# Optimization experiments

Hardware: AMD Instinct MI355X
Metric: run time of the kernel (lower is better)

Reference implementation:

```python
import jax, jax.numpy as jnp
import numpy as np

WBITS = 4   # weight bits (symmetric signed)
ABITS = 4   # activation bits (unsigned, [0,1])
CBITS = 4   # partial-sum quantization bits
ARRAY = 128 # crossbar array size (input-dim tile)
BN_EPS = 1e-5


def ste_round(x):
    # straight-through estimator round (identity gradient)
    return x + jax.lax.stop_gradient(jnp.round(x) - x)


def setup_inputs() -> dict:
    key = jax.random.key(0)
    k1, k2 = jax.random.split(key)
    B, FIN, FOUT = 65536, 256, 256
    x = jax.random.uniform(k1, (B, FIN), dtype=jnp.float32)        # quantized-act range [0,1]
    weight = jax.random.normal(k2, (FOUT, FIN), dtype=jnp.float32) * 0.05
    gamma = jnp.ones((FOUT,), jnp.float32)
    beta = jnp.zeros((FOUT,), jnp.float32)
    return {"x": x, "weight": weight, "gamma": gamma, "beta": beta}


def reference(x, weight, gamma, beta):
    qmax_w = 2 ** (WBITS - 1) - 1          # 7
    qmax_a = 2 ** ABITS - 1                # 15

    # --- symmetric weight quantization to WBITS (integer levels) ---
    scale_w = jnp.max(jnp.abs(weight)) / qmax_w
    w_int = ste_round(jnp.clip(weight / scale_w, -qmax_w, qmax_w))  # [Fout, Fin]

    # --- unsigned activation quantization to ABITS (integer levels) ---
    x_int = ste_round(jnp.clip(x, 0.0, 1.0) * qmax_a)               # [B, Fin]

    # --- crossbar-tiled integer matmul with partial-sum quantization ---
    B, Fin = x.shape
    Fout = weight.shape[0]
    T = Fin // ARRAY
    xt = x_int.reshape(B, T, ARRAY)          # [B, T, A]
    wt = w_int.reshape(Fout, T, ARRAY)       # [Fout, T, A]
    psum = jnp.einsum('bta,ota->bto', xt, wt)  # integer partial sums, [B, T, Fout]

    # quantize each partial sum to CBITS levels over the full tile dynamic range
    pmax = float(ARRAY * qmax_a * qmax_w)
    step = (2.0 * pmax) / (2 ** CBITS - 1)
    psum_q = ste_round(psum / step) * step

    acc = psum_q.sum(axis=1) * (scale_w / qmax_a)   # dequantized linear output [B, Fout]

    # --- BatchNorm1d (training mode: batch statistics) ---
    mu = acc.mean(axis=0)
    var = acc.var(axis=0)
    y = (acc - mu) * jax.lax.rsqrt(var + BN_EPS) * gamma + beta

    # --- quantized clipped-ReLU activation to ABITS ---
    out = ste_round(jnp.clip(y, 0.0, 1.0) * qmax_a) / qmax_a
    return out
```

## Files before the change

kernel.cpp:

```cpp
#include <hip/hip_runtime.h>
#include <cstdint>
#include <cstddef>

typedef int   v4i __attribute__((ext_vector_type(4)));
typedef float v4f __attribute__((ext_vector_type(4)));

static constexpr int NREP = 16;

static constexpr size_t WQ_OFF    = 0;
static constexpr size_t STATS_OFF = 65536;
static constexpr size_t SCALE_OFF = STATS_OFF + NREP*512*4;
static constexpr size_t AB_OFF    = SCALE_OFF + 64;
static constexpr size_t SBUF_OFF  = 131072 + 2048;
static constexpr size_t WS_NEEDED = SBUF_OFF + (size_t)65536 * 256;
static constexpr size_t ZERO_BYTES = NREP*512*4 + 64;

__device__ __forceinline__ int rhe1792(int p) {
    unsigned u = (unsigned)(p + 17024);
    unsigned v = u >> 8;
    unsigned d = (v * 147u) >> 10;
    int q = (int)d - 9;
    unsigned tie = (unsigned)(((u & 255u) | (v - 7u * d)) == 0u);
    q -= (int)(tie & ((unsigned)q & 1u));
    return q;
}

__global__ void k_maxabs(const float* __restrict__ w, unsigned* scalebits) {
    int idx = blockIdx.x * 256 + threadIdx.x;
    float4 f = ((const float4*)w)[idx];
    float m = fmaxf(fmaxf(fabsf(f.x), fabsf(f.y)), fmaxf(fabsf(f.z), fabsf(f.w)));
    #pragma unroll
    for (int s = 32; s > 0; s >>= 1) m = fmaxf(m, __shfl_xor(m, s, 64));
    if ((threadIdx.x & 63) == 0) atomicMax(scalebits, __float_as_uint(m));
}

__global__ void k_wquant(const float* __restrict__ w, const unsigned* __restrict__ scalebits,
                         signed char* __restrict__ wq) {
    int idx = blockIdx.x * 256 + threadIdx.x;
    float scale = __uint_as_float(*scalebits) / 7.0f;
    float4 f = ((const float4*)w)[idx];
    int q0 = (int)rintf(fminf(fmaxf(f.x / scale, -7.f), 7.f));
    int q1 = (int)rintf(fminf(fmaxf(f.y / scale, -7.f), 7.f));
    int q2 = (int)rintf(fminf(fmaxf(f.z / scale, -7.f), 7.f));
    int q3 = (int)rintf(fminf(fmaxf(f.w / scale, -7.f), 7.f));
    ((int*)wq)[idx] = (q0 & 255) | ((q1 & 255) << 8) | ((q2 & 255) << 16) | ((q3 & 255) << 24);
}

template <typename ST>
__global__ __launch_bounds__(256, 3) void k_gemm(
    const float* __restrict__ x, const signed char* __restrict__ wq,
    ST* __restrict__ sbuf, int* __restrict__ stats)
{
    __shared__ __align__(16) signed char ldsx[2][16 * 272];
    const int tid  = threadIdx.x;
    const int lane = tid & 63;
    const int wv   = tid >> 6;
    const int obase = wv * 64;
    const int lr = lane & 15, quad = lane >> 4;

    v4i wf[4][4];
    #pragma unroll
    for (int ot = 0; ot < 4; ++ot)
        #pragma unroll
        for (int kt = 0; kt < 4; ++kt)
            wf[ot][kt] = *(const v4i*)(wq + (size_t)(obase + ot * 16 + lr) * 256 + kt * 64 + quad * 16);

    int ssum[4] = {0, 0, 0, 0};
    int ssq[4]  = {0, 0, 0, 0};

    const int r = tid >> 4, g = tid & 15;
    const int ITER = 4;
    const size_t rb0 = (size_t)blockIdx.x * (16 * ITER);

    v4f f[4];
    {
        const v4f* xr = (const v4f*)(x + (rb0 + r) * 256);
        #pragma unroll
        for (int j = 0; j < 4; ++j) f[j] = __builtin_nontemporal_load(&xr[j * 16 + g]);
    }

    for (int it = 0; it < ITER; ++it) {
        signed char* lb = ldsx[it & 1];
        #pragma unroll
        for (int j = 0; j < 4; ++j) {
            int b0 = (int)rintf(fminf(fmaxf(f[j][0], 0.f), 1.f) * 15.f);
            int b1 = (int)rintf(fminf(fmaxf(f[j][1], 0.f), 1.f) * 15.f);
            int b2 = (int)rintf(fminf(fmaxf(f[j][2], 0.f), 1.f) * 15.f);
            int b3 = (int)rintf(fminf(fmaxf(f[j][3], 0.f), 1.f) * 15.f);
            *(int*)(lb + r * 272 + j * 64 + g * 4) = b0 | (b1 << 8) | (b2 << 16) | (b3 << 24);
        }
        __syncthreads();
        if (it + 1 < ITER) {
            const v4f* xr = (const v4f*)(x + (rb0 + (it + 1) * 16 + r) * 256);
            #pragma unroll
            for (int j = 0; j < 4; ++j) f[j] = __builtin_nontemporal_load(&xr[j * 16 + g]);
        }
        v4i a[4];
        #pragma unroll
        for (int kt = 0; kt < 4; ++kt)
            a[kt] = *(const v4i*)(lb + lr * 272 + kt * 64 + quad * 16);
        const size_t rowbase = rb0 + (size_t)it * 16;
        #pragma unroll
        for (int ot = 0; ot < 4; ++ot) {
            v4i acc0 = {0, 0, 0, 0}, acc1 = {0, 0, 0, 0};
            acc0 = __builtin_amdgcn_mfma_i32_16x16x64_i8(a[0], wf[ot][0], acc0, 0, 0, 0);
            acc0 = __builtin_amdgcn_mfma_i32_16x16x64_i8(a[1], wf[ot][1], acc0, 0, 0, 0);
            acc1 = __builtin_amdgcn_mfma_i32_16x16x64_i8(a[2], wf[ot][2], acc1, 0, 0, 0);
            acc1 = __builtin_amdgcn_mfma_i32_16x16x64_i8(a[3], wf[ot][3], acc1, 0, 0, 0);
            const int ocol = obase + ot * 16 + lr;
            ST* sp = sbuf + (rowbase + quad * 4) * 256 + ocol;
            #pragma unroll
            for (int e = 0; e < 4; ++e) {
                int s = rhe1792(acc0[e]) + rhe1792(acc1[e]);
                ssum[ot] += s;
                ssq[ot]  += s * s;
                sp[(size_t)e * 256] = (ST)s;
            }
        }
    }
    int* st = stats + (blockIdx.x & (NREP - 1)) * 512;
    #pragma unroll
    for (int ot = 0; ot < 4; ++ot) {
        int v = ssum[ot], u = ssq[ot];
        v += __shfl_xor(v, 16, 64); v += __shfl_xor(v, 32, 64);
        u += __shfl_xor(u, 16, 64); u += __shfl_xor(u, 32, 64);
        if (quad == 0) {
            atomicAdd(&st[obase + ot * 16 + lr], v);
            atomicAdd(&st[256 + obase + ot * 16 + lr], u);
        }
    }
}

__global__ void k_stats(const int* __restrict__ stats, const unsigned* __restrict__ scalebits,
                        const float* __restrict__ gamma, const float* __restrict__ beta,
                        float2* __restrict__ AB)
{
    int o = threadIdx.x;
    int s = 0, q = 0;
    #pragma unroll
    for (int rr = 0; rr < NREP; ++rr) {
        s += stats[rr * 512 + o];
        q += stats[rr * 512 + 256 + o];
    }
    float scale_w = __uint_as_float(*scalebits) / 7.0f;
    float t = scale_w / 15.0f;
    double Cs = 1792.0 * (double)t;
    const double N = 65536.0;
    double mean_s = (double)s / N;
    double var_s  = (double)q / N - mean_s * mean_s;
    double var    = Cs * Cs * var_s;
    double inv    = 1.0 / sqrt(var + 1e-5);
    double A = Cs * inv * (double)gamma[o];
    double B = (double)beta[o] - Cs * mean_s * inv * (double)gamma[o];
    AB[o] = make_float2((float)A, (float)B);
}

template <typename LT>
__global__ __launch_bounds__(256) void k_out(const LT* sbuf, const float2* __restrict__ AB,
                                             float* out)
{
    const int tid = threadIdx.x;
    const int o0 = (tid * 4) & 255;
    const float4 ab01 = *(const float4*)((const float*)AB + 2 * o0);
    const float4 ab23 = *(const float4*)((const float*)AB + 2 * o0 + 4);
    const size_t base = (size_t)blockIdx.x * 1024 + tid;
    #pragma unroll
    for (int j = 0; j < 4; ++j) {
        const size_t F4 = base + (size_t)j * 256;
        float v0, v1, v2, v3;
        if constexpr (sizeof(LT) == 1) {
            int sv = ((const int*)sbuf)[F4];
            v0 = (float)((sv << 24) >> 24);
            v1 = (float)((sv << 16) >> 24);
            v2 = (float)((sv << 8) >> 24);
            v3 = (float)(sv >> 24);
        } else {
            v4f fl = ((const v4f*)sbuf)[F4];
            v0 = fl[0]; v1 = fl[1]; v2 = fl[2]; v3 = fl[3];
        }
        float y0 = rintf(fminf(fmaxf(v0 * ab01.x + ab01.y, 0.f), 1.f) * 15.f);
        float y1 = rintf(fminf(fmaxf(v1 * ab01.z + ab01.w, 0.f), 1.f) * 15.f);
        float y2 = rintf(fminf(fmaxf(v2 * ab23.x + ab23.y, 0.f), 1.f) * 15.f);
        float y3 = rintf(fminf(fmaxf(v3 * ab23.z + ab23.w, 0.f), 1.f) * 15.f);
        const float inv15 = 0.066666666666666666f;
        v4f o = { y0 * inv15, y1 * inv15, y2 * inv15, y3 * inv15 };
        __builtin_nontemporal_store(o, (v4f*)out + F4);
    }
}

extern "C" void kernel_launch(void* const* d_in, const int* in_sizes, int n_in,
                              void* d_out, int out_size, void* d_ws, size_t ws_size,
                              hipStream_t stream)
{
    const float* x     = (const float*)d_in[0];
    const float* w     = (const float*)d_in[1];
    const float* gamma = (const float*)d_in[2];
    const float* beta  = (const float*)d_in[3];
    float* out = (float*)d_out;
    char* ws = (char*)d_ws;

    signed char* wq        = (signed char*)(ws + WQ_OFF);
    int*         stats     = (int*)(ws + STATS_OFF);
    unsigned*    scalebits = (unsigned*)(ws + SCALE_OFF);
    float2*      AB        = (float2*)(ws + AB_OFF);

    hipMemsetAsync(ws + STATS_OFF, 0, ZERO_BYTES, stream);
    k_maxabs<<<dim3(64), dim3(256), 0, stream>>>(w, scalebits);
    k_wquant<<<dim3(64), dim3(256), 0, stream>>>(w, scalebits, wq);

    if (ws_size >= WS_NEEDED) {
        signed char* sbuf = (signed char*)(ws + SBUF_OFF);
        k_gemm<signed char><<<dim3(1024), dim3(256), 0, stream>>>(x, wq, sbuf, stats);
        k_stats<<<dim3(1), dim3(256), 0, stream>>>(stats, scalebits, gamma, beta, AB);
        k_out<signed char><<<dim3(4096), dim3(256), 0, stream>>>(sbuf, AB, out);
    } else {
        k_gemm<float><<<dim3(1024), dim3(256), 0, stream>>>(x, wq, out, stats);
        k_stats<<<dim3(1), dim3(256), 0, stream>>>(stats, scalebits, gamma, beta, AB);
        k_out<float><<<dim3(4096), dim3(256), 0, stream>>>(out, AB, out);
    }
}
```

Baseline: 146.4 us.

## Drop memset via in-kernel zeroing and front-load all x loads in GEMM

Replaces the hipMemsetAsync and the atomicMax scale reduction with per-block partial maxima that k_maxabs writes. k_maxabs also zeroes the stats buffer, and k_wquant and k_stats each reduce the 64 partials themselves. The GEMM kernel now issues all 16 float4 loads for its 64 rows up front and quantizes them into one 64-row LDS tile with a single barrier, replacing the double-buffered 16-row pipeline. This removes one stream operation and the per-iteration syncs, at the cost of more registers and LDS per block, which could lower occupancy.

```diff
diff --git a/kernel.cpp b/kernel.cpp
--- a/kernel.cpp
+++ b/kernel.cpp
@@ -9,11 +9,10 @@
 
 static constexpr size_t WQ_OFF    = 0;
 static constexpr size_t STATS_OFF = 65536;
-static constexpr size_t SCALE_OFF = STATS_OFF + NREP*512*4;
-static constexpr size_t AB_OFF    = SCALE_OFF + 64;
+static constexpr size_t PART_OFF  = STATS_OFF + NREP*512*4;
+static constexpr size_t AB_OFF    = PART_OFF + 256;
 static constexpr size_t SBUF_OFF  = 131072 + 2048;
 static constexpr size_t WS_NEEDED = SBUF_OFF + (size_t)65536 * 256;
-static constexpr size_t ZERO_BYTES = NREP*512*4 + 64;
 
 __device__ __forceinline__ int rhe1792(int p) {
     unsigned u = (unsigned)(p + 17024);
@@ -25,19 +24,32 @@
     return q;
 }
 
-__global__ void k_maxabs(const float* __restrict__ w, unsigned* scalebits) {
+__global__ void k_maxabs(const float* __restrict__ w, float* __restrict__ partials,
+                         int* __restrict__ stats) {
+    __shared__ float wmax[4];
     int idx = blockIdx.x * 256 + threadIdx.x;
     float4 f = ((const float4*)w)[idx];
     float m = fmaxf(fmaxf(fabsf(f.x), fabsf(f.y)), fmaxf(fabsf(f.z), fabsf(f.w)));
     #pragma unroll
     for (int s = 32; s > 0; s >>= 1) m = fmaxf(m, __shfl_xor(m, s, 64));
-    if ((threadIdx.x & 63) == 0) atomicMax(scalebits, __float_as_uint(m));
-}
-
-__global__ void k_wquant(const float* __restrict__ w, const unsigned* __restrict__ scalebits,
+    if ((threadIdx.x & 63) == 0) wmax[threadIdx.x >> 6] = m;
+    if (idx < NREP * 512) stats[idx] = 0;
+    __syncthreads();
+    if (threadIdx.x == 0)
+        partials[blockIdx.x] = fmaxf(fmaxf(wmax[0], wmax[1]), fmaxf(wmax[2], wmax[3]));
+}
+
+__device__ __forceinline__ float reduce_partials(const float* __restrict__ partials, int tid) {
+    float p = partials[tid & 63];
+    #pragma unroll
+    for (int s = 32; s > 0; s >>= 1) p = fmaxf(p, __shfl_xor(p, s, 64));
+    return p;
+}
+
+__global__ void k_wquant(const float* __restrict__ w, const float* __restrict__ partials,
                          signed char* __restrict__ wq) {
     int idx = blockIdx.x * 256 + threadIdx.x;
-    float scale = __uint_as_float(*scalebits) / 7.0f;
+    float scale = reduce_partials(partials, threadIdx.x) / 7.0f;
     float4 f = ((const float4*)w)[idx];
     int q0 = (int)rintf(fminf(fmaxf(f.x / scale, -7.f), 7.f));
     int q1 = (int)rintf(fminf(fmaxf(f.y / scale, -7.f), 7.f));
@@ -51,12 +63,19 @@
     const float* __restrict__ x, const signed char* __restrict__ wq,
     ST* __restrict__ sbuf, int* __restrict__ stats)
 {
-    __shared__ __align__(16) signed char ldsx[2][16 * 272];
+    __shared__ __align__(16) signed char ldsx[64 * 272];
     const int tid  = threadIdx.x;
     const int lane = tid & 63;
     const int wv   = tid >> 6;
     const int obase = wv * 64;
     const int lr = lane & 15, quad = lane >> 4;
+    const size_t rb0 = (size_t)blockIdx.x * 64;
+
+    v4f f[16];
+    const v4f* xb = (const v4f*)(x + rb0 * 256);
+    #pragma unroll
+    for (int j = 0; j < 16; ++j)
+        f[j] = __builtin_nontemporal_load(&xb[j * 256 + tid]);
 
     v4i wf[4][4];
     #pragma unroll
@@ -65,41 +84,28 @@
         for (int kt = 0; kt < 4; ++kt)
             wf[ot][kt] = *(const v4i*)(wq + (size_t)(obase + ot * 16 + lr) * 256 + kt * 64 + quad * 16);
 
+    #pragma unroll
+    for (int j = 0; j < 16; ++j) {
+        int idx = j * 256 + tid;
+        int row = idx >> 6, c = idx & 63;
+        int b0 = (int)rintf(fminf(fmaxf(f[j][0], 0.f), 1.f) * 15.f);
+        int b1 = (int)rintf(fminf(fmaxf(f[j][1], 0.f), 1.f) * 15.f);
+        int b2 = (int)rintf(fminf(fmaxf(f[j][2], 0.f), 1.f) * 15.f);
+        int b3 = (int)rintf(fminf(fmaxf(f[j][3], 0.f), 1.f) * 15.f);
+        *(int*)(ldsx + row * 272 + c * 4) = b0 | (b1 << 8) | (b2 << 16) | (b3 << 24);
+    }
+    __syncthreads();
+
     int ssum[4] = {0, 0, 0, 0};
     int ssq[4]  = {0, 0, 0, 0};
 
-    const int r = tid >> 4, g = tid & 15;
-    const int ITER = 4;
-    const size_t rb0 = (size_t)blockIdx.x * (16 * ITER);
-
-    v4f f[4];
-    {
-        const v4f* xr = (const v4f*)(x + (rb0 + r) * 256);
-        #pragma unroll
-        for (int j = 0; j < 4; ++j) f[j] = __builtin_nontemporal_load(&xr[j * 16 + g]);
-    }
-
-    for (int it = 0; it < ITER; ++it) {
-        signed char* lb = ldsx[it & 1];
-        #pragma unroll
-        for (int j = 0; j < 4; ++j) {
-            int b0 = (int)rintf(fminf(fmaxf(f[j][0], 0.f), 1.f) * 15.f);
-            int b1 = (int)rintf(fminf(fmaxf(f[j][1], 0.f), 1.f) * 15.f);
-            int b2 = (int)rintf(fminf(fmaxf(f[j][2], 0.f), 1.f) * 15.f);
-            int b3 = (int)rintf(fminf(fmaxf(f[j][3], 0.f), 1.f) * 15.f);
-            *(int*)(lb + r * 272 + j * 64 + g * 4) = b0 | (b1 << 8) | (b2 << 16) | (b3 << 24);
-        }
-        __syncthreads();
-        if (it + 1 < ITER) {
-            const v4f* xr = (const v4f*)(x + (rb0 + (it + 1) * 16 + r) * 256);
-            #pragma unroll
-            for (int j = 0; j < 4; ++j) f[j] = __builtin_nontemporal_load(&xr[j * 16 + g]);
-        }
+    #pragma unroll
+    for (int t = 0; t < 4; ++t) {
         v4i a[4];
         #pragma unroll
         for (int kt = 0; kt < 4; ++kt)
-            a[kt] = *(const v4i*)(lb + lr * 272 + kt * 64 + quad * 16);
-        const size_t rowbase = rb0 + (size_t)it * 16;
+            a[kt] = *(const v4i*)(ldsx + (t * 16 + lr) * 272 + kt * 64 + quad * 16);
+        const size_t rowbase = rb0 + (size_t)t * 16;
         #pragma unroll
         for (int ot = 0; ot < 4; ++ot) {
             v4i acc0 = {0, 0, 0, 0}, acc1 = {0, 0, 0, 0};
@@ -131,7 +137,7 @@
     }
 }
 
-__global__ void k_stats(const int* __restrict__ stats, const unsigned* __restrict__ scalebits,
+__global__ void k_stats(const int* __restrict__ stats, const float* __restrict__ partials,
                         const float* __restrict__ gamma, const float* __restrict__ beta,
                         float2* __restrict__ AB)
 {
@@ -142,7 +148,7 @@
         s += stats[rr * 512 + o];
         q += stats[rr * 512 + 256 + o];
     }
-    float scale_w = __uint_as_float(*scalebits) / 7.0f;
+    float scale_w = reduce_partials(partials, o) / 7.0f;
     float t = scale_w / 15.0f;
     double Cs = 1792.0 * (double)t;
     const double N = 65536.0;
@@ -199,23 +205,22 @@
     float* out = (float*)d_out;
     char* ws = (char*)d_ws;
 
-    signed char* wq        = (signed char*)(ws + WQ_OFF);
-    int*         stats     = (int*)(ws + STATS_OFF);
-    unsigned*    scalebits = (unsigned*)(ws + SCALE_OFF);
-    float2*      AB        = (float2*)(ws + AB_OFF);
-
-    hipMemsetAsync(ws + STATS_OFF, 0, ZERO_BYTES, stream);
-    k_maxabs<<<dim3(64), dim3(256), 0, stream>>>(w, scalebits);
-    k_wquant<<<dim3(64), dim3(256), 0, stream>>>(w, scalebits, wq);
+    signed char* wq       = (signed char*)(ws + WQ_OFF);
+    int*         stats    = (int*)(ws + STATS_OFF);
+    float*       partials = (float*)(ws + PART_OFF);
+    float2*      AB       = (float2*)(ws + AB_OFF);
+
+    k_maxabs<<<dim3(64), dim3(256), 0, stream>>>(w, partials, stats);
+    k_wquant<<<dim3(64), dim3(256), 0, stream>>>(w, partials, wq);
 
     if (ws_size >= WS_NEEDED) {
         signed char* sbuf = (signed char*)(ws + SBUF_OFF);
         k_gemm<signed char><<<dim3(1024), dim3(256), 0, stream>>>(x, wq, sbuf, stats);
-        k_stats<<<dim3(1), dim3(256), 0, stream>>>(stats, scalebits, gamma, beta, AB);
+        k_stats<<<dim3(1), dim3(256), 0, stream>>>(stats, partials, gamma, beta, AB);
         k_out<signed char><<<dim3(4096), dim3(256), 0, stream>>>(sbuf, AB, out);
     } else {
         k_gemm<float><<<dim3(1024), dim3(256), 0, stream>>>(x, wq, out, stats);
-        k_stats<<<dim3(1), dim3(256), 0, stream>>>(stats, scalebits, gamma, beta, AB);
+        k_stats<<<dim3(1), dim3(256), 0, stream>>>(stats, partials, gamma, beta, AB);
         k_out<float><<<dim3(4096), dim3(256), 0, stream>>>(out, AB, out);
     }
 }
```

New measurement: 142.1 us. -2.9%, faster.
